# Performance work log

Hardware: AMD Instinct MI355X
Metric: run time of the kernel (lower is better)

Reference implementation:

```python
import jax, jax.numpy as jnp
import numpy as np

L, H, NH, NKV, HD, S, P, FF = 2, 2048, 16, 2, 128, 1024, 1024, 5632
G = NH // NKV
THETA = 1000000.0
EPS = 1e-6
SCALE = 1.0 / np.sqrt(HD).astype(np.float32)


def rms_norm(x, w):
    return x * jax.lax.rsqrt(jnp.mean(x * x, axis=-1, keepdims=True) + EPS) * w


def rotate_half(x):
    x1, x2 = jnp.split(x, 2, axis=-1)
    return jnp.concatenate([-x2, x1], axis=-1)


def setup_inputs() -> dict:
    key = jax.random.key(0)
    ks = iter(jax.random.split(key, 16))
    w = lambda shape: jax.random.normal(next(ks), shape, jnp.float32) * 0.02
    return {
        'inputs_embeds': jax.random.normal(next(ks), (1, S, H), jnp.float32),
        'position_ids': (jnp.arange(S, dtype=jnp.int32) + P)[None, :],
        'past_k': jax.random.normal(next(ks), (L, 1, NKV, P, HD), jnp.float32),
        'past_v': jax.random.normal(next(ks), (L, 1, NKV, P, HD), jnp.float32),
        'ln1_w': jnp.ones((L, H), jnp.float32),
        'wq': w((L, H, NH * HD)), 'bq': jnp.zeros((L, NH * HD), jnp.float32),
        'wk': w((L, H, NKV * HD)), 'bk': jnp.zeros((L, NKV * HD), jnp.float32),
        'wv': w((L, H, NKV * HD)), 'bv': jnp.zeros((L, NKV * HD), jnp.float32),
        'wo': w((L, NH * HD, H)),
        'ln2_w': jnp.ones((L, H), jnp.float32),
        'w_gate': w((L, H, FF)), 'w_up': w((L, H, FF)), 'w_down': w((L, FF, H)),
        'norm_w': jnp.ones((H,), jnp.float32),
    }


def reference(inputs_embeds, position_ids, past_k, past_v, ln1_w, wq, bq, wk, bk,
              wv, bv, wo, ln2_w, w_gate, w_up, w_down, norm_w):
    pos = position_ids.astype(jnp.float32)                      # [1,S]
    inv_freq = 1.0 / (THETA ** (jnp.arange(0, HD, 2, dtype=jnp.float32) / HD))
    freqs = pos[:, :, None] * inv_freq                          # [1,S,HD/2]
    emb = jnp.concatenate([freqs, freqs], axis=-1)              # [1,S,HD]
    cos = jnp.cos(emb)[:, None]                                 # [1,1,S,HD]
    sin = jnp.sin(emb)[:, None]
    T = P + S
    k_pos = jnp.arange(T, dtype=jnp.float32)
    # causal mask over absolute positions: future keys masked with -65504
    mask = jnp.where(k_pos[None, None, None, :] > pos[:, None, :, None],
                     jnp.float32(-65504.0), jnp.float32(0.0))   # [1,1,S,T]

    hidden = inputs_embeds
    present = []
    for i in range(L):
        residual = hidden
        h = rms_norm(hidden, ln1_w[i])
        q = (h @ wq[i] + bq[i]).reshape(1, S, NH, HD).transpose(0, 2, 1, 3)
        k = (h @ wk[i] + bk[i]).reshape(1, S, NKV, HD).transpose(0, 2, 1, 3)
        v = (h @ wv[i] + bv[i]).reshape(1, S, NKV, HD).transpose(0, 2, 1, 3)
        q = q * cos + rotate_half(q) * sin
        k = k * cos + rotate_half(k) * sin
        k = jnp.concatenate([past_k[i], k], axis=2)             # [1,NKV,T,HD]
        v = jnp.concatenate([past_v[i], v], axis=2)
        present.append(k)
        present.append(v)
        # GQA: group query heads per kv head instead of expanding k/v
        qg = q.reshape(1, NKV, G, S, HD)
        attn = jnp.einsum('bkgsd,bktd->bkgst', qg, k) * SCALE   # [1,NKV,G,S,T]
        attn = jax.nn.softmax(attn + mask[:, :, None], axis=-1)
        out = jnp.einsum('bkgst,bktd->bkgsd', attn, v)
        out = out.reshape(1, NH, S, HD).transpose(0, 2, 1, 3).reshape(1, S, H)
        hidden = residual + out @ wo[i]
        residual = hidden
        h = rms_norm(hidden, ln2_w[i])
        h = (jax.nn.silu(h @ w_gate[i]) * (h @ w_up[i])) @ w_down[i]
        hidden = residual + h
    hidden = rms_norm(hidden, norm_w)
    return (hidden, *present)
```

## Files before the change

kernel.cpp:

```cpp
#include <hip/hip_runtime.h>

#define L_ 2
#define H_ 2048
#define NH_ 16
#define NKV_ 2
#define HD_ 128
#define S_ 1024
#define P_ 1024
#define T_ 2048
#define FF_ 5632
#define QKVN_ 2560
#define KOFF_ 2048
#define VOFF_ 2304

#define EPS_ 1e-6f
#define SCALE_ 0.08838834764831845f
#define DEFER_THR_ 8.0f

typedef __bf16 bf16_t;
typedef unsigned int u32;
typedef __bf16 bx8 __attribute__((ext_vector_type(8)));
typedef __bf16 bx4 __attribute__((ext_vector_type(4)));
typedef float  fx4 __attribute__((ext_vector_type(4)));

__device__ __forceinline__ fx4 mfma16(bx8 a, bx8 b, fx4 c) {
  return __builtin_amdgcn_mfma_f32_16x16x32_bf16(a, b, c, 0, 0, 0);
}

#define GLL16(gsrc, ldst) __builtin_amdgcn_global_load_lds( \
    (__attribute__((address_space(1))) void*)(gsrc),        \
    (__attribute__((address_space(3))) void*)(ldst), 16, 0, 0)

__device__ __forceinline__ bx8 lds_read_b128(char* p) {
  u32 a = (u32)(uintptr_t)(__attribute__((address_space(3))) void*)p;
  bx8 d;
  asm volatile("ds_read_b128 %0, %1" : "=v"(d) : "v"(a));
  return d;
}
__device__ __forceinline__ void lds_write_b16(char* p, float v) {
  u32 a = (u32)(uintptr_t)(__attribute__((address_space(3))) void*)p;
  bf16_t b = (bf16_t)v;
  u32 d = (u32)__builtin_bit_cast(unsigned short, b);
  asm volatile("ds_write_b16 %0, %1" :: "v"(a), "v"(d));
}

#define LGKM(n) asm volatile("s_waitcnt lgkmcnt(" #n ")" ::: "memory"); __builtin_amdgcn_sched_barrier(0)

__device__ __forceinline__ int xcd_swizzle(int orig, int nwg) {
  int q = nwg >> 3, r = nwg & 7;
  int xcd = orig & 7, lid = orig >> 3;
  return (xcd < r ? xcd * (q + 1) : r * (q + 1) + (xcd - r) * q) + lid;
}

__global__ void k_rope_tables(const int* __restrict__ pos, float* __restrict__ ct, float* __restrict__ st) {
  int i = blockIdx.x * 256 + threadIdx.x;
  if (i >= S_ * 64) return;
  int s = i >> 6, d = i & 63;
  float p = (float)pos[s];
  float inv = expf(-(float)(2 * d) * (13.815510557964274f / 128.0f));
  float f = p * inv;
  ct[i] = cosf(f);
  st[i] = sinf(f);
}

__global__ void k_copy4(const float* __restrict__ in, float* __restrict__ out, int n4) {
  int i = blockIdx.x * 256 + threadIdx.x;
  if (i < n4) ((fx4*)out)[i] = ((const fx4*)in)[i];
}

__global__ void k_cbias(const float* __restrict__ bq, const float* __restrict__ bk,
                        const float* __restrict__ bv, float* __restrict__ cb) {
  int i = blockIdx.x * 256 + threadIdx.x;
  if (i >= L_ * QKVN_) return;
  int l = i / QKVN_, j = i % QKVN_;
  float v;
  if (j < KOFF_)      v = bq[l * KOFF_ + j];
  else if (j < VOFF_) v = bk[l * (NKV_ * HD_) + j - KOFF_];
  else                v = bv[l * (NKV_ * HD_) + j - VOFF_];
  cb[i] = v;
}

template<int OUTBF>
__global__ __launch_bounds__(256) void k_rmsnorm(const float* __restrict__ x, const float* __restrict__ w,
                                                 void* __restrict__ y) {
  int row = blockIdx.x, tid = threadIdx.x;
  const fx4* xr = (const fx4*)(x + (size_t)row * H_);
  fx4 v0 = xr[tid], v1 = xr[tid + 256];
  float ss = v0[0]*v0[0] + v0[1]*v0[1] + v0[2]*v0[2] + v0[3]*v0[3]
           + v1[0]*v1[0] + v1[1]*v1[1] + v1[2]*v1[2] + v1[3]*v1[3];
  #pragma unroll
  for (int off = 32; off > 0; off >>= 1) ss += __shfl_xor(ss, off);
  __shared__ float red[4];
  if ((tid & 63) == 0) red[tid >> 6] = ss;
  __syncthreads();
  float tot = red[0] + red[1] + red[2] + red[3];
  float rs = rsqrtf(tot * (1.0f / H_) + EPS_);
  const fx4* wr_ = (const fx4*)w;
  fx4 w0 = wr_[tid], w1 = wr_[tid + 256];
  if (OUTBF) {
    bf16_t* yb = (bf16_t*)y + (size_t)row * H_;
    bx4 o0, o1;
    #pragma unroll
    for (int i = 0; i < 4; i++) { o0[i] = (bf16_t)(v0[i] * rs * w0[i]); o1[i] = (bf16_t)(v1[i] * rs * w1[i]); }
    *(bx4*)&yb[tid * 4] = o0;
    *(bx4*)&yb[(tid + 256) * 4] = o1;
  } else {
    float* yf = (float*)y + (size_t)row * H_;
    fx4 o0, o1;
    #pragma unroll
    for (int i = 0; i < 4; i++) { o0[i] = v0[i] * rs * w0[i]; o1[i] = v1[i] * rs * w1[i]; }
    *(fx4*)&yf[tid * 4] = o0;
    *(fx4*)&yf[(tid + 256) * 4] = o1;
  }
}

__global__ __launch_bounds__(256) void k_transpose_w(const float* __restrict__ in, bf16_t* __restrict__ out,
                                                     int R, int C) {
  __shared__ __attribute__((aligned(16))) float Tt[64 * 68];
  int tid = threadIdx.x;
  int c0 = blockIdx.x * 64, r0 = blockIdx.y * 64;
  #pragma unroll
  for (int j = 0; j < 4; j++) {
    int c = j * 256 + tid;
    int row = c >> 4, col = (c & 15) * 4;
    *(fx4*)&Tt[row * 68 + col] = *(const fx4*)&in[(size_t)(r0 + row) * C + c0 + col];
  }
  __syncthreads();
  #pragma unroll
  for (int j = 0; j < 2; j++) {
    int c = j * 256 + tid;
    int n = c >> 3, ko = (c & 7) * 8;
    bx8 o;
    #pragma unroll
    for (int i = 0; i < 8; i++) o[i] = (bf16_t)Tt[(ko + i) * 68 + n];
    *(bx8*)&out[(size_t)(c0 + n) * R + r0 + ko] = o;
  }
}

template<int OUTBF, int HASB, int HASR, int HASG>
__global__ __launch_bounds__(256) void k_gemm(const bf16_t* __restrict__ A, const bf16_t* __restrict__ Bt,
                                              const float* __restrict__ bias, const float* __restrict__ res,
                                              const bf16_t* __restrict__ gmul,
                                              void* __restrict__ out, int M, int N, int K, int gy) {
  __shared__ __attribute__((aligned(16))) bf16_t sA[3][64 * 64];
  __shared__ __attribute__((aligned(16))) bf16_t sB[3][128 * 64];
  int tid = threadIdx.x;
  int w = tid >> 6, lane = tid & 63, g = lane >> 4, r = lane & 15;
  int wr = w >> 1, wc = w & 1;
  int swzid = xcd_swizzle((int)blockIdx.x, (int)gridDim.x);
  int m0 = (swzid % gy) * 64;
  int n0 = (swzid / gy) * 128;
  fx4 acc[2][4] = {};
  int swz = (r & 7) << 4;
  int col0 = (g * 16) ^ swz;
  int col1 = (64 + g * 16) ^ swz;
  int wbase = (tid & ~63) * 16;
  int nk = K >> 6;

  auto STAGE = [&](int buf, int k0) {
    #pragma unroll
    for (int j = 0; j < 2; j++) {
      int d = (j * 256 + tid) * 16;
      int row = d >> 7;
      int inrow = (d & 127) ^ ((row & 7) << 4);
      GLL16((const char*)(A + (size_t)(m0 + row) * K + k0) + inrow,
            (char*)&sA[buf][0] + j * 4096 + wbase);
    }
    #pragma unroll
    for (int j = 0; j < 4; j++) {
      int d = (j * 256 + tid) * 16;
      int row = d >> 7;
      int inrow = (d & 127) ^ ((row & 7) << 4);
      GLL16((const char*)(Bt + (size_t)(n0 + row) * K + k0) + inrow,
            (char*)&sB[buf][0] + j * 4096 + wbase);
    }
  };

  STAGE(0, 0);
  STAGE(1, 64);
  asm volatile("s_waitcnt vmcnt(6)" ::: "memory");
  __builtin_amdgcn_s_barrier();
  __builtin_amdgcn_sched_barrier(0);
  int cur = 0;
  for (int t = 0; t < nk; t++) {
    if (t + 2 < nk) STAGE((cur + 2) % 3, (t + 2) << 6);
    char* pa = (char*)&sA[cur][0] + (wr * 32 + r) * 128;
    char* pb = (char*)&sB[cur][0] + (wc * 64 + r) * 128;
    bx8 fa[2][2], fb[4][2];
    fa[0][0] = lds_read_b128(pa + col0);
    fa[1][0] = lds_read_b128(pa + 2048 + col0);
    #pragma unroll
    for (int n = 0; n < 4; n++) fb[n][0] = lds_read_b128(pb + n * 2048 + col0);
    fa[0][1] = lds_read_b128(pa + col1);
    fa[1][1] = lds_read_b128(pa + 2048 + col1);
    #pragma unroll
    for (int n = 0; n < 4; n++) fb[n][1] = lds_read_b128(pb + n * 2048 + col1);
    LGKM(6);
    __builtin_amdgcn_s_setprio(1);
    #pragma unroll
    for (int n = 0; n < 4; n++) {
      acc[0][n] = mfma16(fa[0][0], fb[n][0], acc[0][n]);
      acc[1][n] = mfma16(fa[1][0], fb[n][0], acc[1][n]);
    }
    __builtin_amdgcn_s_setprio(0);
    LGKM(0);
    __builtin_amdgcn_s_setprio(1);
    #pragma unroll
    for (int n = 0; n < 4; n++) {
      acc[0][n] = mfma16(fa[0][1], fb[n][1], acc[0][n]);
      acc[1][n] = mfma16(fa[1][1], fb[n][1], acc[1][n]);
    }
    __builtin_amdgcn_s_setprio(0);
    if (t + 1 < nk) {
      if (t + 2 < nk) { asm volatile("s_waitcnt vmcnt(6)" ::: "memory"); }
      else            { asm volatile("s_waitcnt vmcnt(0)" ::: "memory"); }
      __builtin_amdgcn_s_barrier();
      __builtin_amdgcn_sched_barrier(0);
    }
    cur = (cur + 1) % 3;
  }
  #pragma unroll
  for (int m = 0; m < 2; m++)
    #pragma unroll
    for (int n = 0; n < 4; n++) {
      int col = n0 + wc * 64 + n * 16 + r;
      #pragma unroll
      for (int rr = 0; rr < 4; rr++) {
        int row = m0 + wr * 32 + m * 16 + 4 * g + rr;
        float v = acc[m][n][rr];
        if (HASB) v += bias[col];
        if (HASR) v += res[(size_t)row * N + col];
        if (HASG) {
          float x = (float)gmul[(size_t)row * N + col];
          v = (x / (1.0f + __expf(-x))) * v;
        }
        if (OUTBF) ((bf16_t*)out)[(size_t)row * N + col] = (bf16_t)v;
        else       ((float*)out)[(size_t)row * N + col] = v;
      }
    }
}

__global__ void k_rope_q(const bf16_t* __restrict__ qkv, const float* __restrict__ ct,
                         const float* __restrict__ st, bf16_t* __restrict__ qout) {
  int i = blockIdx.x * 256 + threadIdx.x;
  if (i >= S_ * NH_ * 64) return;
  int d = i & 63, h = (i >> 6) & 15, s = i >> 10;
  size_t ib = (size_t)s * QKVN_ + h * HD_;
  float x1 = (float)qkv[ib + d];
  float x2 = (float)qkv[ib + d + 64];
  float c = ct[s * 64 + d], sn = st[s * 64 + d];
  size_t ob = ((size_t)h * S_ + s) * HD_;
  qout[ob + d]      = (bf16_t)(x1 * c - x2 * sn);
  qout[ob + d + 64] = (bf16_t)(x2 * c + x1 * sn);
}

__global__ void k_build_k(const bf16_t* __restrict__ qkv, const float* __restrict__ pastk,
                          const float* __restrict__ ct, const float* __restrict__ st,
                          bf16_t* __restrict__ kc, float* __restrict__ pk_out) {
  int i = blockIdx.x * 256 + threadIdx.x;
  if (i >= NKV_ * T_ * 64) return;
  int d = i & 63, t = (i >> 6) & (T_ - 1), kv = i >> 17;
  size_t cb = ((size_t)kv * T_ + t) * HD_;
  if (t < P_) {
    size_t pb = ((size_t)kv * P_ + t) * HD_;
    float a = pastk[pb + d], b = pastk[pb + d + 64];
    kc[cb + d] = (bf16_t)a; kc[cb + d + 64] = (bf16_t)b;
    pk_out[cb + d] = a;     pk_out[cb + d + 64] = b;
  } else {
    int s = t - P_;
    size_t ib = (size_t)s * QKVN_ + KOFF_ + kv * HD_;
    float x1 = (float)qkv[ib + d];
    float x2 = (float)qkv[ib + d + 64];
    float c = ct[s * 64 + d], sn = st[s * 64 + d];
    float k1 = x1 * c - x2 * sn, k2 = x2 * c + x1 * sn;
    kc[cb + d] = (bf16_t)k1; kc[cb + d + 64] = (bf16_t)k2;
    pk_out[cb + d] = k1;     pk_out[cb + d + 64] = k2;
  }
}

__global__ __launch_bounds__(256) void k_build_vt(const bf16_t* __restrict__ qkv, const float* __restrict__ pastv,
                                                  bf16_t* __restrict__ vt, float* __restrict__ pv_out) {
  int t0 = blockIdx.x * 64, d0 = blockIdx.y * 64, kv = blockIdx.z;
  __shared__ __attribute__((aligned(16))) float Tt[64 * 68];
  int tid = threadIdx.x;
  if (t0 < P_) {
    #pragma unroll
    for (int j = 0; j < 4; j++) {
      int c = j * 256 + tid;
      int row = c >> 4, col = (c & 15) * 4;
      int t = t0 + row;
      fx4 v = *(const fx4*)&pastv[((size_t)kv * P_ + t) * HD_ + d0 + col];
      *(fx4*)&Tt[row * 68 + col] = v;
      *(fx4*)&pv_out[((size_t)kv * T_ + t) * HD_ + d0 + col] = v;
    }
  } else {
    #pragma unroll
    for (int j = 0; j < 4; j++) {
      int c = j * 256 + tid;
      int row = c >> 4, col = (c & 15) * 4;
      int t = t0 + row;
      bx4 b = *(const bx4*)&qkv[(size_t)(t - P_) * QKVN_ + VOFF_ + kv * HD_ + d0 + col];
      fx4 v;
      #pragma unroll
      for (int q = 0; q < 4; q++) v[q] = (float)b[q];
      *(fx4*)&Tt[row * 68 + col] = v;
      *(fx4*)&pv_out[((size_t)kv * T_ + t) * HD_ + d0 + col] = v;
    }
  }
  __syncthreads();
  #pragma unroll
  for (int j = 0; j < 2; j++) {
    int c = j * 256 + tid;
    int n = c >> 3, ko = (c & 7) * 8;
    bx8 o;
    #pragma unroll
    for (int i = 0; i < 8; i++) o[i] = (bf16_t)Tt[(ko + i) * 68 + n];
    *(bx8*)&vt[((size_t)kv * HD_ + d0 + n) * T_ + t0 + ko] = o;
  }
}

__global__ __launch_bounds__(128) void k_attn(const bf16_t* __restrict__ Q, const bf16_t* __restrict__ Kc,
                                              const bf16_t* __restrict__ VT, bf16_t* __restrict__ O) {
  __shared__ __attribute__((aligned(16))) bf16_t Klds[2][64 * 128];
  __shared__ __attribute__((aligned(16))) bf16_t Vlds[2][128 * 64];
  __shared__ __attribute__((aligned(16))) bf16_t Plds[2][16][72];
  int tid = threadIdx.x;
  int w = tid >> 6, lane = tid & 63, g = lane >> 4, r = lane & 15;
  int b = blockIdx.x;
  int half = b >> 8;
  int idx = b & 255;
  int cx = idx & 31;
  int chunk = half ? (31 - cx) : cx;
  int h = (half << 3) | (idx >> 5);
  int kv = half;
  int m0 = chunk * 32;
  int qr0 = m0 + w * 16;
  const bf16_t* qb = Q + ((size_t)h * S_ + qr0 + r) * HD_ + g * 8;
  bx8 qf[4];
  #pragma unroll
  for (int kc = 0; kc < 4; kc++) qf[kc] = *(const bx8*)(qb + kc * 32);
  fx4 of[8] = {};
  float mrun[4], lrun[4];
  #pragma unroll
  for (int i = 0; i < 4; i++) { mrun[i] = -1e30f; lrun[i] = 0.0f; }
  int lim = P_ + qr0 + 4 * g;
  int ntile = (P_ + m0 + 32 + 63) >> 6;
  const char* kg = (const char*)(Kc + (size_t)kv * T_ * HD_);
  const char* vg = (const char*)(VT + (size_t)kv * HD_ * T_);
  int wbase = (tid & ~63) * 16;

  auto STAGE = [&](int buf, int t0) {
    #pragma unroll
    for (int j = 0; j < 8; j++) {
      int D = j * 2048 + tid * 16;
      int row = D >> 8, inrow = D & 255;
      const char* src = kg + (size_t)(t0 + row) * 256 + (inrow ^ ((row & 7) << 4));
      GLL16(src, (char*)&Klds[buf][0] + j * 2048 + wbase);
    }
    #pragma unroll
    for (int j = 0; j < 8; j++) {
      int D = j * 2048 + tid * 16;
      int row = D >> 7, inrow = D & 127;
      const char* src = vg + (size_t)row * 4096 + (size_t)t0 * 2 + (inrow ^ ((row & 7) << 4));
      GLL16(src, (char*)&Vlds[buf][0] + j * 2048 + wbase);
    }
  };

  STAGE(0, 0);
  asm volatile("s_waitcnt vmcnt(0)" ::: "memory");
  __builtin_amdgcn_s_barrier();
  __builtin_amdgcn_sched_barrier(0);
  int cur = 0;
  for (int t = 0; t < ntile; t++) {
    int t0 = t * 64;
    if (t + 1 < ntile) {
      STAGE(cur ^ 1, t0 + 64);
      asm volatile("s_waitcnt vmcnt(16)" ::: "memory");
    } else {
      asm volatile("s_waitcnt vmcnt(0)" ::: "memory");
    }
    __builtin_amdgcn_s_barrier();
    __builtin_amdgcn_sched_barrier(0);
    char* kb = (char*)&Klds[cur][0];
    bx8 kf[4][4];
    #pragma unroll
    for (int nt = 0; nt < 4; nt++) {
      int row = nt * 16 + r;
      char* kr = kb + row * 256;
      int sz = (row & 7) << 4;
      #pragma unroll
      for (int kc = 0; kc < 4; kc++)
        kf[nt][kc] = lds_read_b128(kr + (((kc * 32 + g * 8) * 2) ^ sz));
    }
    fx4 sc[4] = {};
    LGKM(12);
    #pragma unroll
    for (int kc = 0; kc < 4; kc++) sc[0] = mfma16(qf[kc], kf[0][kc], sc[0]);
    LGKM(8);
    #pragma unroll
    for (int kc = 0; kc < 4; kc++) sc[1] = mfma16(qf[kc], kf[1][kc], sc[1]);
    LGKM(4);
    #pragma unroll
    for (int kc = 0; kc < 4; kc++) sc[2] = mfma16(qf[kc], kf[2][kc], sc[2]);
    LGKM(0);
    #pragma unroll
    for (int kc = 0; kc < 4; kc++) sc[3] = mfma16(qf[kc], kf[3][kc], sc[3]);
    float lm[4] = {-1e30f, -1e30f, -1e30f, -1e30f};
    #pragma unroll
    for (int nt = 0; nt < 4; nt++)
      #pragma unroll
      for (int rr = 0; rr < 4; rr++) {
        int key = t0 + nt * 16 + r;
        float sv = sc[nt][rr] * SCALE_;
        sv = (key > lim + rr) ? -1e30f : sv;
        sc[nt][rr] = sv;
        lm[rr] = fmaxf(lm[rr], sv);
      }
    int ok = (lm[0] <= mrun[0] + DEFER_THR_) & (lm[1] <= mrun[1] + DEFER_THR_) &
             (lm[2] <= mrun[2] + DEFER_THR_) & (lm[3] <= mrun[3] + DEFER_THR_);
    if (!__all(ok)) {
      float av[4];
      #pragma unroll
      for (int off = 1; off < 16; off <<= 1)
        #pragma unroll
        for (int rr = 0; rr < 4; rr++) lm[rr] = fmaxf(lm[rr], __shfl_xor(lm[rr], off));
      #pragma unroll
      for (int rr = 0; rr < 4; rr++) {
        float mn = fmaxf(mrun[rr], lm[rr]);
        av[rr] = __expf(mrun[rr] - mn);
        mrun[rr] = mn;
        lrun[rr] *= av[rr];
      }
      #pragma unroll
      for (int f = 0; f < 8; f++)
        #pragma unroll
        for (int rr = 0; rr < 4; rr++) of[f][rr] *= av[rr];
    }
    #pragma unroll
    for (int nt = 0; nt < 4; nt++)
      #pragma unroll
      for (int rr = 0; rr < 4; rr++) {
        float pr = __expf(sc[nt][rr] - mrun[rr]);
        lrun[rr] += pr;
        lds_write_b16((char*)&Plds[w][4 * g + rr][nt * 16 + r], pr);
      }
    LGKM(0);
    char* vb = (char*)&Vlds[cur][0];
    bx8 pa0 = lds_read_b128((char*)&Plds[w][r][g * 8]);
    bx8 vf0[8], vf1[8];
    #pragma unroll
    for (int dt = 0; dt < 8; dt++) {
      int row = dt * 16 + r;
      vf0[dt] = lds_read_b128(vb + row * 128 + (((g * 8) * 2) ^ ((row & 7) << 4)));
    }
    bx8 pa1 = lds_read_b128((char*)&Plds[w][r][32 + g * 8]);
    #pragma unroll
    for (int dt = 0; dt < 8; dt++) {
      int row = dt * 16 + r;
      vf1[dt] = lds_read_b128(vb + row * 128 + (((32 + g * 8) * 2) ^ ((row & 7) << 4)));
    }
    LGKM(9);
    #pragma unroll
    for (int dt = 0; dt < 8; dt++) of[dt] = mfma16(pa0, vf0[dt], of[dt]);
    LGKM(0);
    #pragma unroll
    for (int dt = 0; dt < 8; dt++) of[dt] = mfma16(pa1, vf1[dt], of[dt]);
    __builtin_amdgcn_s_barrier();
    cur ^= 1;
  }
  #pragma unroll
  for (int off = 1; off < 16; off <<= 1)
    #pragma unroll
    for (int rr = 0; rr < 4; rr++) lrun[rr] += __shfl_xor(lrun[rr], off);
  float li[4];
  #pragma unroll
  for (int rr = 0; rr < 4; rr++) li[rr] = 1.0f / lrun[rr];
  #pragma unroll
  for (int dt = 0; dt < 8; dt++)
    #pragma unroll
    for (int rr = 0; rr < 4; rr++)
      O[(size_t)(qr0 + 4 * g + rr) * H_ + h * HD_ + dt * 16 + r] = (bf16_t)(of[dt][rr] * li[rr]);
}

extern "C" void kernel_launch(void* const* d_in, const int* in_sizes, int n_in,
                              void* d_out, int out_size, void* d_ws, size_t ws_size,
                              hipStream_t stream) {
  const float* embeds = (const float*)d_in[0];
  const int*   pos    = (const int*)d_in[1];
  const float* past_k = (const float*)d_in[2];
  const float* past_v = (const float*)d_in[3];
  const float* ln1    = (const float*)d_in[4];
  const float* wq     = (const float*)d_in[5];
  const float* bq     = (const float*)d_in[6];
  const float* wk     = (const float*)d_in[7];
  const float* bk     = (const float*)d_in[8];
  const float* wv     = (const float*)d_in[9];
  const float* bv     = (const float*)d_in[10];
  const float* wo     = (const float*)d_in[11];
  const float* ln2    = (const float*)d_in[12];
  const float* wg     = (const float*)d_in[13];
  const float* wu     = (const float*)d_in[14];
  const float* wd     = (const float*)d_in[15];
  const float* normw  = (const float*)d_in[16];

  char* wsp = (char*)d_ws;
  auto take = [&](size_t n) { char* p = wsp; wsp += (n + 255) & ~(size_t)255; return (void*)p; };
  float*  cos_t  = (float*)take((size_t)S_ * 64 * 4);
  float*  sin_t  = (float*)take((size_t)S_ * 64 * 4);
  float*  cbias  = (float*)take((size_t)L_ * QKVN_ * 4);
  float*  hidden = (float*)take((size_t)S_ * H_ * 4);
  bf16_t* hnorm  = (bf16_t*)take((size_t)S_ * H_ * 2);
  bf16_t* qkv    = (bf16_t*)take((size_t)S_ * QKVN_ * 2);
  bf16_t* qrope  = (bf16_t*)take((size_t)NH_ * S_ * HD_ * 2);
  bf16_t* kcache = (bf16_t*)take((size_t)NKV_ * T_ * HD_ * 2);
  bf16_t* vtr    = (bf16_t*)take((size_t)NKV_ * HD_ * T_ * 2);
  bf16_t* attno  = (bf16_t*)take((size_t)S_ * H_ * 2);
  bf16_t* gateb  = (bf16_t*)take((size_t)S_ * FF_ * 2);
  bf16_t* hgb    = (bf16_t*)take((size_t)S_ * FF_ * 2);
  bf16_t* wT     = (bf16_t*)take((size_t)FF_ * H_ * 2);

  float* out_h = (float*)d_out;

  k_rope_tables<<<256, 256, 0, stream>>>(pos, cos_t, sin_t);
  k_cbias<<<(L_ * QKVN_ + 255) / 256, 256, 0, stream>>>(bq, bk, bv, cbias);
  k_copy4<<<(S_ * H_ / 4 + 255) / 256, 256, 0, stream>>>(embeds, hidden, S_ * H_ / 4);

  for (int l = 0; l < L_; l++) {
    const float* wq_l = wq + (size_t)l * H_ * (NH_ * HD_);
    const float* wk_l = wk + (size_t)l * H_ * (NKV_ * HD_);
    const float* wv_l = wv + (size_t)l * H_ * (NKV_ * HD_);
    const float* wo_l = wo + (size_t)l * (NH_ * HD_) * H_;
    const float* wg_l = wg + (size_t)l * H_ * FF_;
    const float* wu_l = wu + (size_t)l * H_ * FF_;
    const float* wd_l = wd + (size_t)l * FF_ * H_;
    const float* pk_in = past_k + (size_t)l * NKV_ * P_ * HD_;
    const float* pv_in = past_v + (size_t)l * NKV_ * P_ * HD_;
    float* pk_out = out_h + (size_t)S_ * H_ + (size_t)l * 2 * NKV_ * T_ * HD_;
    float* pv_out = pk_out + (size_t)NKV_ * T_ * HD_;

    k_rmsnorm<1><<<S_, 256, 0, stream>>>(hidden, ln1 + (size_t)l * H_, hnorm);
    k_transpose_w<<<dim3(32, 32), 256, 0, stream>>>(wq_l, wT, H_, NH_ * HD_);
    k_transpose_w<<<dim3(4, 32), 256, 0, stream>>>(wk_l, wT + (size_t)KOFF_ * H_, H_, NKV_ * HD_);
    k_transpose_w<<<dim3(4, 32), 256, 0, stream>>>(wv_l, wT + (size_t)VOFF_ * H_, H_, NKV_ * HD_);
    k_gemm<1, 1, 0, 0><<<(QKVN_ / 128) * (S_ / 64), 256, 0, stream>>>(
        hnorm, wT, cbias + (size_t)l * QKVN_, nullptr, nullptr, qkv, S_, QKVN_, H_, S_ / 64);
    k_rope_q<<<(S_ * NH_ * 64) / 256, 256, 0, stream>>>(qkv, cos_t, sin_t, qrope);
    k_build_k<<<(NKV_ * T_ * 64) / 256, 256, 0, stream>>>(qkv, pk_in, cos_t, sin_t, kcache, pk_out);
    k_build_vt<<<dim3(T_ / 64, HD_ / 64, NKV_), 256, 0, stream>>>(qkv, pv_in, vtr, pv_out);
    k_attn<<<512, 128, 0, stream>>>(qrope, kcache, vtr, attno);
    k_transpose_w<<<dim3(32, 32), 256, 0, stream>>>(wo_l, wT, NH_ * HD_, H_);
    k_gemm<0, 0, 1, 0><<<(H_ / 128) * (S_ / 64), 256, 0, stream>>>(
        attno, wT, nullptr, hidden, nullptr, hidden, S_, H_, NH_ * HD_, S_ / 64);
    k_rmsnorm<1><<<S_, 256, 0, stream>>>(hidden, ln2 + (size_t)l * H_, hnorm);
    k_transpose_w<<<dim3(88, 32), 256, 0, stream>>>(wg_l, wT, H_, FF_);
    k_gemm<1, 0, 0, 0><<<(FF_ / 128) * (S_ / 64), 256, 0, stream>>>(
        hnorm, wT, nullptr, nullptr, nullptr, gateb, S_, FF_, H_, S_ / 64);
    k_transpose_w<<<dim3(88, 32), 256, 0, stream>>>(wu_l, wT, H_, FF_);
    k_gemm<1, 0, 0, 1><<<(FF_ / 128) * (S_ / 64), 256, 0, stream>>>(
        hnorm, wT, nullptr, nullptr, gateb, hgb, S_, FF_, H_, S_ / 64);
    k_transpose_w<<<dim3(32, 88), 256, 0, stream>>>(wd_l, wT, FF_, H_);
    k_gemm<0, 0, 1, 0><<<(H_ / 128) * (S_ / 64), 256, 0, stream>>>(
        hgb, wT, nullptr, hidden, nullptr, hidden, S_, H_, FF_, S_ / 64);
  }
  k_rmsnorm<0><<<S_, 256, 0, stream>>>(hidden, normw, out_h);
}
```

Measured before the change: 569.5 us.

## Split-K the down projection with atomic accumulation and double-buffer GEMM staging

The down-projection GEMM (K=5632) is split into two K halves launched as twice as many blocks, and each half atomically adds its partial result into the fp32 hidden buffer, which already holds the residual. The intent is to fill more CUs than the 256 blocks of the original grid. The GEMM pipeline also changes from a three-stage LDS ring to double buffering with a barrier at the top of each iteration, which lowers LDS use but may expose more load latency. Atomics add memory traffic and make the summation order nondeterministic.

```diff
diff --git a/kernel.cpp b/kernel.cpp
--- a/kernel.cpp
+++ b/kernel.cpp
@@ -137,25 +137,30 @@
   }
 }
 
-template<int OUTBF, int HASB, int HASR, int HASG>
+template<int OUTBF, int HASB, int HASR, int HASG, int SPLIT>
 __global__ __launch_bounds__(256) void k_gemm(const bf16_t* __restrict__ A, const bf16_t* __restrict__ Bt,
                                               const float* __restrict__ bias, const float* __restrict__ res,
                                               const bf16_t* __restrict__ gmul,
-                                              void* __restrict__ out, int M, int N, int K, int gy) {
-  __shared__ __attribute__((aligned(16))) bf16_t sA[3][64 * 64];
-  __shared__ __attribute__((aligned(16))) bf16_t sB[3][128 * 64];
+                                              void* __restrict__ out, int M, int N, int lda, int kLen, int gy) {
+  __shared__ __attribute__((aligned(16))) bf16_t sA[2][64 * 64];
+  __shared__ __attribute__((aligned(16))) bf16_t sB[2][128 * 64];
   int tid = threadIdx.x;
   int w = tid >> 6, lane = tid & 63, g = lane >> 4, r = lane & 15;
   int wr = w >> 1, wc = w & 1;
   int swzid = xcd_swizzle((int)blockIdx.x, (int)gridDim.x);
-  int m0 = (swzid % gy) * 64;
-  int n0 = (swzid / gy) * 128;
+  int per = (int)gridDim.x / SPLIT;
+  int sp = swzid / per;
+  int rem = swzid - sp * per;
+  int m0 = (rem % gy) * 64;
+  int n0 = (rem / gy) * 128;
+  A  += (size_t)sp * kLen;
+  Bt += (size_t)sp * kLen;
   fx4 acc[2][4] = {};
   int swz = (r & 7) << 4;
   int col0 = (g * 16) ^ swz;
   int col1 = (64 + g * 16) ^ swz;
   int wbase = (tid & ~63) * 16;
-  int nk = K >> 6;
+  int nk = kLen >> 6;
 
   auto STAGE = [&](int buf, int k0) {
     #pragma unroll
@@ -163,7 +168,7 @@
       int d = (j * 256 + tid) * 16;
       int row = d >> 7;
       int inrow = (d & 127) ^ ((row & 7) << 4);
-      GLL16((const char*)(A + (size_t)(m0 + row) * K + k0) + inrow,
+      GLL16((const char*)(A + (size_t)(m0 + row) * lda + k0) + inrow,
             (char*)&sA[buf][0] + j * 4096 + wbase);
     }
     #pragma unroll
@@ -171,19 +176,22 @@
       int d = (j * 256 + tid) * 16;
       int row = d >> 7;
       int inrow = (d & 127) ^ ((row & 7) << 4);
-      GLL16((const char*)(Bt + (size_t)(n0 + row) * K + k0) + inrow,
+      GLL16((const char*)(Bt + (size_t)(n0 + row) * lda + k0) + inrow,
             (char*)&sB[buf][0] + j * 4096 + wbase);
     }
   };
 
   STAGE(0, 0);
-  STAGE(1, 64);
-  asm volatile("s_waitcnt vmcnt(6)" ::: "memory");
-  __builtin_amdgcn_s_barrier();
-  __builtin_amdgcn_sched_barrier(0);
   int cur = 0;
   for (int t = 0; t < nk; t++) {
-    if (t + 2 < nk) STAGE((cur + 2) % 3, (t + 2) << 6);
+    if (t + 1 < nk) {
+      STAGE(cur ^ 1, (t + 1) << 6);
+      asm volatile("s_waitcnt vmcnt(6)" ::: "memory");
+    } else {
+      asm volatile("s_waitcnt vmcnt(0)" ::: "memory");
+    }
+    __builtin_amdgcn_s_barrier();
+    __builtin_amdgcn_sched_barrier(0);
     char* pa = (char*)&sA[cur][0] + (wr * 32 + r) * 128;
     char* pb = (char*)&sB[cur][0] + (wc * 64 + r) * 128;
     bx8 fa[2][2], fb[4][2];
@@ -212,12 +220,10 @@
     }
     __builtin_amdgcn_s_setprio(0);
     if (t + 1 < nk) {
-      if (t + 2 < nk) { asm volatile("s_waitcnt vmcnt(6)" ::: "memory"); }
-      else            { asm volatile("s_waitcnt vmcnt(0)" ::: "memory"); }
       __builtin_amdgcn_s_barrier();
       __builtin_amdgcn_sched_barrier(0);
     }
-    cur = (cur + 1) % 3;
+    cur ^= 1;
   }
   #pragma unroll
   for (int m = 0; m < 2; m++)
@@ -228,14 +234,18 @@
       for (int rr = 0; rr < 4; rr++) {
         int row = m0 + wr * 32 + m * 16 + 4 * g + rr;
         float v = acc[m][n][rr];
-        if (HASB) v += bias[col];
-        if (HASR) v += res[(size_t)row * N + col];
-        if (HASG) {
-          float x = (float)gmul[(size_t)row * N + col];
-          v = (x / (1.0f + __expf(-x))) * v;
+        if (SPLIT > 1) {
+          atomicAdd(&((float*)out)[(size_t)row * N + col], v);
+        } else {
+          if (HASB) v += bias[col];
+          if (HASR) v += res[(size_t)row * N + col];
+          if (HASG) {
+            float x = (float)gmul[(size_t)row * N + col];
+            v = (x / (1.0f + __expf(-x))) * v;
+          }
+          if (OUTBF) ((bf16_t*)out)[(size_t)row * N + col] = (bf16_t)v;
+          else       ((float*)out)[(size_t)row * N + col] = v;
         }
-        if (OUTBF) ((bf16_t*)out)[(size_t)row * N + col] = (bf16_t)v;
-        else       ((float*)out)[(size_t)row * N + col] = v;
       }
     }
 }
@@ -542,25 +552,25 @@
     k_transpose_w<<<dim3(32, 32), 256, 0, stream>>>(wq_l, wT, H_, NH_ * HD_);
     k_transpose_w<<<dim3(4, 32), 256, 0, stream>>>(wk_l, wT + (size_t)KOFF_ * H_, H_, NKV_ * HD_);
     k_transpose_w<<<dim3(4, 32), 256, 0, stream>>>(wv_l, wT + (size_t)VOFF_ * H_, H_, NKV_ * HD_);
-    k_gemm<1, 1, 0, 0><<<(QKVN_ / 128) * (S_ / 64), 256, 0, stream>>>(
-        hnorm, wT, cbias + (size_t)l * QKVN_, nullptr, nullptr, qkv, S_, QKVN_, H_, S_ / 64);
+    k_gemm<1, 1, 0, 0, 1><<<(QKVN_ / 128) * (S_ / 64), 256, 0, stream>>>(
+        hnorm, wT, cbias + (size_t)l * QKVN_, nullptr, nullptr, qkv, S_, QKVN_, H_, H_, S_ / 64);
     k_rope_q<<<(S_ * NH_ * 64) / 256, 256, 0, stream>>>(qkv, cos_t, sin_t, qrope);
     k_build_k<<<(NKV_ * T_ * 64) / 256, 256, 0, stream>>>(qkv, pk_in, cos_t, sin_t, kcache, pk_out);
     k_build_vt<<<dim3(T_ / 64, HD_ / 64, NKV_), 256, 0, stream>>>(qkv, pv_in, vtr, pv_out);
     k_attn<<<512, 128, 0, stream>>>(qrope, kcache, vtr, attno);
     k_transpose_w<<<dim3(32, 32), 256, 0, stream>>>(wo_l, wT, NH_ * HD_, H_);
-    k_gemm<0, 0, 1, 0><<<(H_ / 128) * (S_ / 64), 256, 0, stream>>>(
-        attno, wT, nullptr, hidden, nullptr, hidden, S_, H_, NH_ * HD_, S_ / 64);
+    k_gemm<0, 0, 1, 0, 1><<<(H_ / 128) * (S_ / 64), 256, 0, stream>>>(
+        attno, wT, nullptr, hidden, nullptr, hidden, S_, H_, NH_ * HD_, NH_ * HD_, S_ / 64);
     k_rmsnorm<1><<<S_, 256, 0, stream>>>(hidden, ln2 + (size_t)l * H_, hnorm);
     k_transpose_w<<<dim3(88, 32), 256, 0, stream>>>(wg_l, wT, H_, FF_);
-    k_gemm<1, 0, 0, 0><<<(FF_ / 128) * (S_ / 64), 256, 0, stream>>>(
-        hnorm, wT, nullptr, nullptr, nullptr, gateb, S_, FF_, H_, S_ / 64);
+    k_gemm<1, 0, 0, 0, 1><<<(FF_ / 128) * (S_ / 64), 256, 0, stream>>>(
+        hnorm, wT, nullptr, nullptr, nullptr, gateb, S_, FF_, H_, H_, S_ / 64);
     k_transpose_w<<<dim3(88, 32), 256, 0, stream>>>(wu_l, wT, H_, FF_);
-    k_gemm<1, 0, 0, 1><<<(FF_ / 128) * (S_ / 64), 256, 0, stream>>>(
-        hnorm, wT, nullptr, nullptr, gateb, hgb, S_, FF_, H_, S_ / 64);
+    k_gemm<1, 0, 0, 1, 1><<<(FF_ / 128) * (S_ / 64), 256, 0, stream>>>(
+        hnorm, wT, nullptr, nullptr, gateb, hgb, S_, FF_, H_, H_, S_ / 64);
     k_transpose_w<<<dim3(32, 88), 256, 0, stream>>>(wd_l, wT, FF_, H_);
-    k_gemm<0, 0, 1, 0><<<(H_ / 128) * (S_ / 64), 256, 0, stream>>>(
-        hgb, wT, nullptr, hidden, nullptr, hidden, S_, H_, FF_, S_ / 64);
+    k_gemm<0, 0, 0, 0, 2><<<2 * (H_ / 128) * (S_ / 64), 256, 0, stream>>>(
+        hgb, wT, nullptr, nullptr, nullptr, hidden, S_, H_, FF_, FF_ / 2, S_ / 64);
   }
   k_rmsnorm<0><<<S_, 256, 0, stream>>>(hidden, normw, out_h);
 }
```

Result: faster. 555.4 us (-2.5%).
